# Optimization experiments

Measured on AMD Instinct MI355X. Metric: run time of the kernel, lower is better.

Reference implementation:

```python
import jax, jax.numpy as jnp
import numpy as np

B, T, D, H, L = 4, 128, 768, 770, 40  # batch, token_num, bert dim, head hidden, n_labels


def setup_inputs() -> dict:
    key = jax.random.key(0)
    ks = jax.random.split(key, 7)
    hidden = jax.random.normal(ks[0], (B, T + 1, D), dtype=jnp.float32)
    pred_spans = jnp.sort(jax.random.randint(ks[1], (B, 2), 0, T), axis=1)
    span_avail = jax.random.randint(ks[2], (T, T), 0, 2).astype(jnp.int32)
    # torch nn.Linear: weight init N(0, 0.02), bias init N(0, 1) (normal_(bias, 0) -> mean=0, std=1)
    W1 = (jax.random.normal(ks[3], (2 * D + 1, H)) * 0.02).astype(jnp.float32)
    b1 = jax.random.normal(ks[4], (H,), dtype=jnp.float32)
    W2 = (jax.random.normal(ks[5], (H, L)) * 0.02).astype(jnp.float32)
    b2 = jax.random.normal(ks[6], (L,), dtype=jnp.float32)
    return {"hidden": hidden, "W1": W1, "b1": b1, "W2": W2, "b2": b2,
            "pred_spans": pred_spans, "span_avail": span_avail, "token_num": T}


def reference(hidden, W1, b1, W2, b2, pred_spans, span_avail, token_num):
    # vecs[i] = hidden[:, i+1, :]  (skip [CLS])
    vecs = hidden[:, 1:token_num + 1, :]                      # [B, T, D]
    Bv, Tv, Dv = vecs.shape
    starts = pred_spans[:, 0][:, None, None]                  # [B,1,1]
    ends = pred_spans[:, 1][:, None, None]
    ii = jnp.arange(Tv)[:, None]                              # [T,1]
    jj = jnp.arange(Tv)[None, :]                              # [1,T]
    # indication: 2 if (i,j) == pred span; 1 if strictly inside span with i<=j; else 0
    is_full = (ii == starts) & (jj == ends)                   # [B,T,T]
    inside = (starts <= ii) & (ii <= jj) & (jj <= ends) & (~is_full)
    ind = (2 * is_full + inside).astype(hidden.dtype)         # [B,T,T]
    fi = jnp.broadcast_to(vecs[:, :, None, :], (Bv, Tv, Tv, Dv))
    fj = jnp.broadcast_to(vecs[:, None, :, :], (Bv, Tv, Tv, Dv))
    feat = jnp.concatenate([fi, fj, ind[..., None]], axis=-1)  # [B,T,T,2D+1]
    h = jax.nn.relu(feat @ W1 + b1)                            # [B,T,T,H]
    out = h @ W2 + b2                                          # [B,T,T,L]
    # unavailable spans contribute a zeros row (original appends `zeros`)
    mask = (span_avail >= 1)[None, :, :, None]
    out = jnp.where(mask, out, jnp.zeros((), out.dtype))
    out = out.reshape(Bv, Tv * Tv, -1)                         # span index c = i*T + j
    return jax.nn.log_softmax(out, axis=1)
```

## Files before the change

### kernel.cpp

```cpp
#include <hip/hip_runtime.h>
#include <math.h>

#define BB 4
#define TT 128
#define DD 768
#define HD 770
#define HP 800
#define LL 40
#define TP1 129

typedef __attribute__((ext_vector_type(8))) short s16x8;
typedef __attribute__((ext_vector_type(4))) float f32x4;

#define P_OFF   0
#define Q_OFF   409600
#define W2F_OFF 819200
#define BF1_OFF 838400
#define ACC_OFF 1440512

__device__ __forceinline__ unsigned pkbf(float a, float b) {
    unsigned ua = __float_as_uint(a);
    unsigned ub = __float_as_uint(b);
    return ((ua + 0x8000u) >> 16) | ((ub + 0x8000u) & 0xffff0000u);
}
__device__ __forceinline__ unsigned rne1(float v) {
    unsigned x = __float_as_uint(v);
    return (x + 0x7fffu + ((x >> 16) & 1u)) >> 16;
}

__global__ __launch_bounds__(256) void kPrep(const float* __restrict__ W1,
                                             const float* __restrict__ W2,
                                             float* __restrict__ Q,
                                             unsigned* __restrict__ W2f,
                                             unsigned* __restrict__ Bf1,
                                             float* __restrict__ accum) {
    const int bx = blockIdx.x;
    const int tid = threadIdx.x;
    if (bx < 19) {
        int u = bx * 256 + tid;
        if (u >= 4800) return;
        int nt = u / 1600;
        int rem = u - nt * 1600;
        int ks = rem >> 6;
        int lane = rem & 63;
        int kbase = ks * 32 + ((lane >> 4) << 3);
        int l = nt * 16 + (lane & 15);
        unsigned pk[4];
        #pragma unroll
        for (int sp = 0; sp < 4; ++sp) {
            unsigned w[2];
            #pragma unroll
            for (int e = 0; e < 2; ++e) {
                int k = kbase + 2 * sp + e;
                float v = (k < HD && l < LL) ? W2[k * LL + l] : 0.0f;
                w[e] = rne1(v);
            }
            pk[sp] = w[0] | (w[1] << 16);
        }
        ((uint4*)W2f)[u] = make_uint4(pk[0], pk[1], pk[2], pk[3]);
    } else if (bx < 607) {
        int u = (bx - 19) * 256 + tid;
        int lane = u & 63;
        int g = u >> 6;
        int ks = g % 24;
        int g2 = g / 24;
        int nt = g2 % 49;
        int half = g2 / 49;
        int kbase = ks * 32 + ((lane >> 4) << 3);
        int h = nt * 16 + (lane & 15);
        int row0 = half * DD + kbase;
        unsigned pk[4];
        #pragma unroll
        for (int sp = 0; sp < 4; ++sp) {
            unsigned w[2];
            #pragma unroll
            for (int e = 0; e < 2; ++e) {
                float v = (h < HD) ? W1[(size_t)(row0 + 2 * sp + e) * HD + h] : 0.0f;
                w[e] = rne1(v);
            }
            pk[sp] = w[0] | (w[1] << 16);
        }
        ((uint4*)Bf1)[u] = make_uint4(pk[0], pk[1], pk[2], pk[3]);
    } else {
        int u = (bx - 607) * 256 + tid;
        if (u < 160) accum[u] = 0.0f;
        int u2 = u - 160;
        if (u2 >= 0 && u2 < 512 * 30) {
            int row = u2 / 30;
            int h = HD + (u2 - row * 30);
            Q[(size_t)row * HP + h] = 0.0f;
        }
    }
}

__global__ __launch_bounds__(256) void kA(const float* __restrict__ hidden,
                                          const unsigned* __restrict__ Bf1,
                                          const float* __restrict__ b1,
                                          float* __restrict__ P,
                                          float* __restrict__ Q) {
    const int tid = threadIdx.x;
    const int w = blockIdx.x * 4 + (tid >> 6);
    const int lane = tid & 63;
    const int mband = w & 31;
    const int nt = w >> 5;
    const int b  = mband >> 3;
    const int tt = mband & 7;

    const float* __restrict__ Arow =
        hidden + (size_t)(b * TP1 + 1 + tt * 16 + (lane & 15)) * DD + ((lane >> 4) << 3);
    const uint4* __restrict__ B0 = (const uint4*)Bf1 + ((size_t)nt * 24) * 64 + lane;
    const uint4* __restrict__ B1 = (const uint4*)Bf1 + ((size_t)(49 + nt) * 24) * 64 + lane;

    f32x4 a0 = (f32x4){0.f,0.f,0.f,0.f};
    f32x4 a1 = (f32x4){0.f,0.f,0.f,0.f};

    #pragma unroll 4
    for (int ks = 0; ks < 24; ++ks) {
        float4 x0 = *(const float4*)(Arow + ks * 32);
        float4 x1 = *(const float4*)(Arow + ks * 32 + 4);
        union { unsigned u[4]; s16x8 v; } af;
        af.u[0] = pkbf(x0.x, x0.y); af.u[1] = pkbf(x0.z, x0.w);
        af.u[2] = pkbf(x1.x, x1.y); af.u[3] = pkbf(x1.z, x1.w);
        union { uint4 q; s16x8 v; } bf0, bf1;
        bf0.q = B0[ks * 64];
        bf1.q = B1[ks * 64];
        a0 = __builtin_amdgcn_mfma_f32_16x16x32_bf16(af.v, bf0.v, a0, 0, 0, 0);
        a1 = __builtin_amdgcn_mfma_f32_16x16x32_bf16(af.v, bf1.v, a1, 0, 0, 0);
    }

    const int col = lane & 15;
    const int h = nt * 16 + col;
    if (h < HD) {
        const float bv = b1[h];
        const int quad = lane >> 4;
        #pragma unroll
        for (int r = 0; r < 4; ++r) {
            int t = tt * 16 + quad * 4 + r;
            size_t row = (size_t)(b * TT + t) * HP;
            P[row + h] = a0[r] + bv;
            Q[row + h] = a1[r];
        }
    }
}

__global__ __launch_bounds__(256) void kB(const float* __restrict__ P,
                                          const float* __restrict__ Q,
                                          const float* __restrict__ W1,
                                          const unsigned* __restrict__ Bfrag,
                                          const float* __restrict__ b2,
                                          const int* __restrict__ spans,
                                          const int* __restrict__ avail,
                                          float* __restrict__ out,
                                          float* __restrict__ accum) {
    __shared__ unsigned Sb[2][128 * 20];
    __shared__ float var[3 * HP];
    __shared__ int avi[TT];
    __shared__ float sred[192];

    const int i = blockIdx.x;
    const int b = blockIdx.y;
    const int tid = threadIdx.x;
    const int wave = tid >> 6;
    const int lane = tid & 63;

    const int start = spans[b * 2];
    const int end   = spans[b * 2 + 1];

    const int jS = tid >> 1;
    const int hh = (tid & 1) << 4;
    int indS;
    {
        bool isfull = (i == start) && (jS == end);
        bool inside = (start <= i) && (i <= jS) && (jS <= end) && !isfull;
        indS = isfull ? 2 : (inside ? 1 : 0);
    }

    {
        const float* Pi  = P + (size_t)(b * TT + i) * HP;
        const float* w1L = W1 + (size_t)2 * DD * HD;
        for (int h = tid; h < HP; h += 256) {
            float pv = (h < HD) ? Pi[h] : 0.0f;
            float wv = (h < HD) ? w1L[h] : 0.0f;
            var[h]          = pv;
            var[HP + h]     = pv + wv;
            var[2*HP + h]   = pv + wv + wv;
        }
        if (tid < TT) avi[tid] = avail[i * TT + tid];
    }
    __syncthreads();

    const float* Qj = Q + (size_t)(b * TT + jS) * HP;
    const float* vb = var + indS * HP;

    auto form = [&](int c, int p) {
        const int h0 = c * 32 + hh;
        const float4* qp = (const float4*)(Qj + h0);
        float4 q0 = qp[0], q1 = qp[1], q2 = qp[2], q3 = qp[3];
        const float4* vp = (const float4*)(vb + h0);
        float4 v0 = vp[0], v1 = vp[1], v2 = vp[2], v3 = vp[3];
        float s0 = fmaxf(v0.x + q0.x, 0.f), s1 = fmaxf(v0.y + q0.y, 0.f);
        float s2 = fmaxf(v0.z + q0.z, 0.f), s3 = fmaxf(v0.w + q0.w, 0.f);
        float s4 = fmaxf(v1.x + q1.x, 0.f), s5 = fmaxf(v1.y + q1.y, 0.f);
        float s6 = fmaxf(v1.z + q1.z, 0.f), s7 = fmaxf(v1.w + q1.w, 0.f);
        float s8 = fmaxf(v2.x + q2.x, 0.f), s9 = fmaxf(v2.y + q2.y, 0.f);
        float sa = fmaxf(v2.z + q2.z, 0.f), sb_ = fmaxf(v2.w + q2.w, 0.f);
        float sc = fmaxf(v3.x + q3.x, 0.f), sd = fmaxf(v3.y + q3.y, 0.f);
        float se = fmaxf(v3.z + q3.z, 0.f), sf = fmaxf(v3.w + q3.w, 0.f);
        uint4* dst = (uint4*)(&Sb[p][jS * 20 + (hh >> 1)]);
        dst[0] = make_uint4(pkbf(s0,s1), pkbf(s2,s3), pkbf(s4,s5), pkbf(s6,s7));
        dst[1] = make_uint4(pkbf(s8,s9), pkbf(sa,sb_), pkbf(sc,sd), pkbf(se,sf));
    };

    f32x4 acc[2][3];
    #pragma unroll
    for (int mt = 0; mt < 2; ++mt)
        #pragma unroll
        for (int nt = 0; nt < 3; ++nt)
            acc[mt][nt] = (f32x4){0.f, 0.f, 0.f, 0.f};

    form(0, 0);
    __syncthreads();

    const int arow0 = (wave * 32 + (lane & 15)) * 20 + ((lane >> 4) << 2);
    for (int c = 0; c < 25; ++c) {
        const int p = c & 1;
        s16x8 bf0 = *(const s16x8*)(Bfrag + (( 0 + c) * 64 + lane) * 4);
        s16x8 bf1 = *(const s16x8*)(Bfrag + ((25 + c) * 64 + lane) * 4);
        s16x8 bf2 = *(const s16x8*)(Bfrag + ((50 + c) * 64 + lane) * 4);
        s16x8 af0 = *(const s16x8*)(&Sb[p][arow0]);
        s16x8 af1 = *(const s16x8*)(&Sb[p][arow0 + 16 * 20]);
        if (c + 1 < 25) form(c + 1, p ^ 1);
        acc[0][0] = __builtin_amdgcn_mfma_f32_16x16x32_bf16(af0, bf0, acc[0][0], 0, 0, 0);
        acc[0][1] = __builtin_amdgcn_mfma_f32_16x16x32_bf16(af0, bf1, acc[0][1], 0, 0, 0);
        acc[0][2] = __builtin_amdgcn_mfma_f32_16x16x32_bf16(af0, bf2, acc[0][2], 0, 0, 0);
        acc[1][0] = __builtin_amdgcn_mfma_f32_16x16x32_bf16(af1, bf0, acc[1][0], 0, 0, 0);
        acc[1][1] = __builtin_amdgcn_mfma_f32_16x16x32_bf16(af1, bf1, acc[1][1], 0, 0, 0);
        acc[1][2] = __builtin_amdgcn_mfma_f32_16x16x32_bf16(af1, bf2, acc[1][2], 0, 0, 0);
        __syncthreads();
    }

    float bias[3];
    #pragma unroll
    for (int nt = 0; nt < 3; ++nt) {
        int l = nt * 16 + (lane & 15);
        bias[nt] = (l < LL) ? b2[l] : 0.0f;
    }
    const int jr0 = wave * 32 + ((lane >> 4) << 2);
    float sE[3] = {0.f, 0.f, 0.f};
    #pragma unroll
    for (int mt = 0; mt < 2; ++mt) {
        #pragma unroll
        for (int r = 0; r < 4; ++r) {
            int j = jr0 + mt * 16 + r;
            bool msk = avi[j] >= 1;
            size_t rowoff = ((size_t)(b * (TT * TT) + i * TT + j)) * LL;
            #pragma unroll
            for (int nt = 0; nt < 3; ++nt) {
                int l = nt * 16 + (lane & 15);
                if (l < LL) {
                    float val = msk ? (acc[mt][nt][r] + bias[nt]) : 0.0f;
                    out[rowoff + l] = val;
                    sE[nt] += __expf(val);
                }
            }
        }
    }
    #pragma unroll
    for (int nt = 0; nt < 3; ++nt) {
        float v = sE[nt];
        v += __shfl_xor(v, 16);
        v += __shfl_xor(v, 32);
        if (lane < 16) sred[wave * 48 + nt * 16 + lane] = v;
    }
    __syncthreads();
    if (tid < 48) {
        float t4 = sred[tid] + sred[48 + tid] + sred[96 + tid] + sred[144 + tid];
        if (tid < LL) atomicAdd(&accum[b * LL + tid], t4);
    }
}

__global__ __launch_bounds__(256) void kD(float* __restrict__ out,
                                          const float* __restrict__ accum) {
    const int idx = blockIdx.x * 256 + threadIdx.x;
    const int e = idx * 4;
    const int b = e / (TT * TT * LL);
    const int l = e % LL;
    float4 v = ((float4*)out)[idx];
    const float* ac = accum + b * LL + l;
    v.x -= __logf(ac[0]); v.y -= __logf(ac[1]);
    v.z -= __logf(ac[2]); v.w -= __logf(ac[3]);
    ((float4*)out)[idx] = v;
}

extern "C" void kernel_launch(void* const* d_in, const int* in_sizes, int n_in,
                              void* d_out, int out_size, void* d_ws, size_t ws_size,
                              hipStream_t stream) {
    const float* hidden = (const float*)d_in[0];
    const float* W1     = (const float*)d_in[1];
    const float* b1     = (const float*)d_in[2];
    const float* W2     = (const float*)d_in[3];
    const float* b2     = (const float*)d_in[4];
    const int*   spans  = (const int*)d_in[5];
    const int*   avail  = (const int*)d_in[6];
    float* out = (float*)d_out;
    float* ws  = (float*)d_ws;

    float*    P     = ws + P_OFF;
    float*    Q     = ws + Q_OFF;
    unsigned* W2f   = (unsigned*)(ws + W2F_OFF);
    unsigned* Bf1   = (unsigned*)(ws + BF1_OFF);
    float*    accum = ws + ACC_OFF;

    kPrep<<<dim3(668),     dim3(256), 0, stream>>>(W1, W2, Q, W2f, Bf1, accum);
    kA   <<<dim3(392),     dim3(256), 0, stream>>>(hidden, Bf1, b1, P, Q);
    kB   <<<dim3(TT, BB),  dim3(256), 0, stream>>>(P, Q, W1, W2f, b2, spans, avail, out, accum);
    kD   <<<dim3(2560),    dim3(256), 0, stream>>>(out, accum);
}
```

Before: 128.6 us.

## Fuse prep, projection, head and log-softmax into one cooperative kernel

Replaces the four separate kernel launches with a single cooperative kernel of 512 blocks that uses grid-wide syncs between the weight-prep, first-projection, head GEMM and log-softmax normalisation phases. It also pre-converts the hidden activations to bf16 fragments in a workspace buffer, so the projection phase loads packed bf16 instead of converting fp32 inline. The aim is to remove launch gaps and per-kernel tail effects. In exchange, every block must stay co-resident, which the 256,2 launch bounds are meant to allow, and grid syncs add barrier cost while idle waves wait in the phases that use fewer blocks.

```diff
diff --git a/kernel.cpp b/kernel.cpp
--- a/kernel.cpp
+++ b/kernel.cpp
@@ -1,5 +1,8 @@
 #include <hip/hip_runtime.h>
+#include <hip/hip_cooperative_groups.h>
 #include <math.h>
+
+namespace cg = cooperative_groups;
 
 #define BB 4
 #define TT 128
@@ -16,7 +19,8 @@
 #define Q_OFF   409600
 #define W2F_OFF 819200
 #define BF1_OFF 838400
-#define ACC_OFF 1440512
+#define AF_OFF  1440512
+#define ACC_OFF 1637120
 
 __device__ __forceinline__ unsigned pkbf(float a, float b) {
     unsigned ua = __float_as_uint(a);
@@ -28,23 +32,77 @@
     return (x + 0x7fffu + ((x >> 16) & 1u)) >> 16;
 }
 
-__global__ __launch_bounds__(256) void kPrep(const float* __restrict__ W1,
-                                             const float* __restrict__ W2,
-                                             float* __restrict__ Q,
-                                             unsigned* __restrict__ W2f,
-                                             unsigned* __restrict__ Bf1,
-                                             float* __restrict__ accum) {
-    const int bx = blockIdx.x;
-    const int tid = threadIdx.x;
-    if (bx < 19) {
-        int u = bx * 256 + tid;
-        if (u >= 4800) return;
-        int nt = u / 1600;
-        int rem = u - nt * 1600;
+__global__ __launch_bounds__(256, 2) void kFused(
+    const float* __restrict__ hidden, const float* __restrict__ W1,
+    const float* __restrict__ W2, const float* __restrict__ b1,
+    const float* __restrict__ b2, const int* __restrict__ spans,
+    const int* __restrict__ avail, float* __restrict__ out,
+    float* __restrict__ ws)
+{
+    __shared__ unsigned Sb[2][128 * 20];
+    __shared__ float var[3 * HP];
+    __shared__ int avi[TT];
+    __shared__ float sred[192];
+
+    cg::grid_group grid = cg::this_grid();
+
+    float*    P     = ws + P_OFF;
+    float*    Q     = ws + Q_OFF;
+    unsigned* W2f   = (unsigned*)(ws + W2F_OFF);
+    unsigned* Bf1   = (unsigned*)(ws + BF1_OFF);
+    unsigned* Af    = (unsigned*)(ws + AF_OFF);
+    float*    accum = ws + ACC_OFF;
+
+    const int tid  = threadIdx.x;
+    const int g    = blockIdx.x * 256 + tid;
+    const int wave = tid >> 6;
+    const int lane = tid & 63;
+
+    for (int u = g; u < 150528; u += 131072) {
+        int ln = u & 63;
+        int gi = u >> 6;
+        int ks = gi % 24;
+        int g2 = gi / 24;
+        int nt = g2 % 49;
+        int half = g2 / 49;
+        int kbase = ks * 32 + ((ln >> 4) << 3);
+        int h = nt * 16 + (ln & 15);
+        int row0 = half * DD + kbase;
+        unsigned pk[4];
+        #pragma unroll
+        for (int sp = 0; sp < 4; ++sp) {
+            unsigned w[2];
+            #pragma unroll
+            for (int e = 0; e < 2; ++e) {
+                float v = (h < HD) ? W1[(size_t)(row0 + 2 * sp + e) * HD + h] : 0.0f;
+                w[e] = rne1(v);
+            }
+            pk[sp] = w[0] | (w[1] << 16);
+        }
+        ((uint4*)Bf1)[u] = make_uint4(pk[0], pk[1], pk[2], pk[3]);
+    }
+    if (g < 49152) {
+        int ln = g & 63;
+        int fi = g >> 6;
+        int ks = fi % 24;
+        int mband = fi / 24;
+        int b = mband >> 3;
+        int tt = mband & 7;
+        int m = ln & 15;
+        int kb = ks * 32 + ((ln >> 4) << 3);
+        const float* src = hidden + (size_t)(b * TP1 + 1 + tt * 16 + m) * DD + kb;
+        float4 x0 = ((const float4*)src)[0];
+        float4 x1 = ((const float4*)src)[1];
+        ((uint4*)Af)[g] = make_uint4(pkbf(x0.x, x0.y), pkbf(x0.z, x0.w),
+                                     pkbf(x1.x, x1.y), pkbf(x1.z, x1.w));
+    }
+    if (g < 4800) {
+        int nt = g / 1600;
+        int rem = g - nt * 1600;
         int ks = rem >> 6;
-        int lane = rem & 63;
-        int kbase = ks * 32 + ((lane >> 4) << 3);
-        int l = nt * 16 + (lane & 15);
+        int ln = rem & 63;
+        int kbase = ks * 32 + ((ln >> 4) << 3);
+        int l = nt * 16 + (ln & 15);
         unsigned pk[4];
         #pragma unroll
         for (int sp = 0; sp < 4; ++sp) {
@@ -57,239 +115,193 @@
             }
             pk[sp] = w[0] | (w[1] << 16);
         }
-        ((uint4*)W2f)[u] = make_uint4(pk[0], pk[1], pk[2], pk[3]);
-    } else if (bx < 607) {
-        int u = (bx - 19) * 256 + tid;
-        int lane = u & 63;
-        int g = u >> 6;
-        int ks = g % 24;
-        int g2 = g / 24;
-        int nt = g2 % 49;
-        int half = g2 / 49;
-        int kbase = ks * 32 + ((lane >> 4) << 3);
-        int h = nt * 16 + (lane & 15);
-        int row0 = half * DD + kbase;
-        unsigned pk[4];
-        #pragma unroll
-        for (int sp = 0; sp < 4; ++sp) {
-            unsigned w[2];
+        ((uint4*)W2f)[g] = make_uint4(pk[0], pk[1], pk[2], pk[3]);
+    }
+    if (g < 16384) {
+        int row = g >> 5;
+        Q[(size_t)row * HP + 768 + (g & 31)] = 0.0f;
+    }
+    if (g < 160) accum[g] = 0.0f;
+
+    grid.sync();
+
+    {
+        const int gw = blockIdx.x * 4 + wave;
+        if (gw < 1568) {
+            const int mband = gw & 31;
+            const int nt = gw >> 5;
+            const int b = mband >> 3;
+            const int tt = mband & 7;
+
+            const uint4* __restrict__ A0 = (const uint4*)Af + (size_t)mband * 24 * 64 + lane;
+            const uint4* __restrict__ B0 = (const uint4*)Bf1 + ((size_t)nt * 24) * 64 + lane;
+            const uint4* __restrict__ B1 = (const uint4*)Bf1 + ((size_t)(49 + nt) * 24) * 64 + lane;
+
+            f32x4 a0 = (f32x4){0.f, 0.f, 0.f, 0.f};
+            f32x4 a1 = (f32x4){0.f, 0.f, 0.f, 0.f};
+
+            #pragma unroll 4
+            for (int ks = 0; ks < 24; ++ks) {
+                union { uint4 q; s16x8 v; } af, bf0, bf1;
+                af.q  = A0[ks * 64];
+                bf0.q = B0[ks * 64];
+                bf1.q = B1[ks * 64];
+                a0 = __builtin_amdgcn_mfma_f32_16x16x32_bf16(af.v, bf0.v, a0, 0, 0, 0);
+                a1 = __builtin_amdgcn_mfma_f32_16x16x32_bf16(af.v, bf1.v, a1, 0, 0, 0);
+            }
+
+            const int col = lane & 15;
+            const int h = nt * 16 + col;
+            if (h < HD) {
+                const float bv = b1[h];
+                const int quad = lane >> 4;
+                #pragma unroll
+                for (int r = 0; r < 4; ++r) {
+                    int t = tt * 16 + quad * 4 + r;
+                    size_t row = (size_t)(b * TT + t) * HP;
+                    P[row + h] = a0[r] + bv;
+                    Q[row + h] = a1[r];
+                }
+            }
+        }
+    }
+
+    grid.sync();
+
+    {
+        const int i = blockIdx.x & 127;
+        const int b = blockIdx.x >> 7;
+
+        const int start = spans[b * 2];
+        const int end   = spans[b * 2 + 1];
+
+        const int jS = tid >> 1;
+        const int hh = (tid & 1) << 4;
+        int indS;
+        {
+            bool isfull = (i == start) && (jS == end);
+            bool inside = (start <= i) && (i <= jS) && (jS <= end) && !isfull;
+            indS = isfull ? 2 : (inside ? 1 : 0);
+        }
+
+        {
+            const float* Pi  = P + (size_t)(b * TT + i) * HP;
+            const float* w1L = W1 + (size_t)2 * DD * HD;
+            for (int h = tid; h < HP; h += 256) {
+                float pv = (h < HD) ? Pi[h] : 0.0f;
+                float wv = (h < HD) ? w1L[h] : 0.0f;
+                var[h]        = pv;
+                var[HP + h]   = pv + wv;
+                var[2*HP + h] = pv + wv + wv;
+            }
+            if (tid < TT) avi[tid] = avail[i * TT + tid];
+        }
+        __syncthreads();
+
+        const float* Qj = Q + (size_t)(b * TT + jS) * HP;
+        const float* vb = var + indS * HP;
+
+        auto form = [&](int c, int p) {
+            const int h0 = c * 32 + hh;
+            const float4* qp = (const float4*)(Qj + h0);
+            float4 q0 = qp[0], q1 = qp[1], q2 = qp[2], q3 = qp[3];
+            const float4* vp = (const float4*)(vb + h0);
+            float4 v0 = vp[0], v1 = vp[1], v2 = vp[2], v3 = vp[3];
+            float s0 = fmaxf(v0.x + q0.x, 0.f), s1 = fmaxf(v0.y + q0.y, 0.f);
+            float s2 = fmaxf(v0.z + q0.z, 0.f), s3 = fmaxf(v0.w + q0.w, 0.f);
+            float s4 = fmaxf(v1.x + q1.x, 0.f), s5 = fmaxf(v1.y + q1.y, 0.f);
+            float s6 = fmaxf(v1.z + q1.z, 0.f), s7 = fmaxf(v1.w + q1.w, 0.f);
+            float s8 = fmaxf(v2.x + q2.x, 0.f), s9 = fmaxf(v2.y + q2.y, 0.f);
+            float sa = fmaxf(v2.z + q2.z, 0.f), sb_ = fmaxf(v2.w + q2.w, 0.f);
+            float sc = fmaxf(v3.x + q3.x, 0.f), sd = fmaxf(v3.y + q3.y, 0.f);
+            float se = fmaxf(v3.z + q3.z, 0.f), sf = fmaxf(v3.w + q3.w, 0.f);
+            uint4* dst = (uint4*)(&Sb[p][jS * 20 + (hh >> 1)]);
+            dst[0] = make_uint4(pkbf(s0,s1), pkbf(s2,s3), pkbf(s4,s5), pkbf(s6,s7));
+            dst[1] = make_uint4(pkbf(s8,s9), pkbf(sa,sb_), pkbf(sc,sd), pkbf(se,sf));
+        };
+
+        f32x4 acc[2][3];
+        #pragma unroll
+        for (int mt = 0; mt < 2; ++mt)
             #pragma unroll
-            for (int e = 0; e < 2; ++e) {
-                float v = (h < HD) ? W1[(size_t)(row0 + 2 * sp + e) * HD + h] : 0.0f;
-                w[e] = rne1(v);
-            }
-            pk[sp] = w[0] | (w[1] << 16);
-        }
-        ((uint4*)Bf1)[u] = make_uint4(pk[0], pk[1], pk[2], pk[3]);
-    } else {
-        int u = (bx - 607) * 256 + tid;
-        if (u < 160) accum[u] = 0.0f;
-        int u2 = u - 160;
-        if (u2 >= 0 && u2 < 512 * 30) {
-            int row = u2 / 30;
-            int h = HD + (u2 - row * 30);
-            Q[(size_t)row * HP + h] = 0.0f;
-        }
-    }
-}
-
-__global__ __launch_bounds__(256) void kA(const float* __restrict__ hidden,
-                                          const unsigned* __restrict__ Bf1,
-                                          const float* __restrict__ b1,
-                                          float* __restrict__ P,
-                                          float* __restrict__ Q) {
-    const int tid = threadIdx.x;
-    const int w = blockIdx.x * 4 + (tid >> 6);
-    const int lane = tid & 63;
-    const int mband = w & 31;
-    const int nt = w >> 5;
-    const int b  = mband >> 3;
-    const int tt = mband & 7;
-
-    const float* __restrict__ Arow =
-        hidden + (size_t)(b * TP1 + 1 + tt * 16 + (lane & 15)) * DD + ((lane >> 4) << 3);
-    const uint4* __restrict__ B0 = (const uint4*)Bf1 + ((size_t)nt * 24) * 64 + lane;
-    const uint4* __restrict__ B1 = (const uint4*)Bf1 + ((size_t)(49 + nt) * 24) * 64 + lane;
-
-    f32x4 a0 = (f32x4){0.f,0.f,0.f,0.f};
-    f32x4 a1 = (f32x4){0.f,0.f,0.f,0.f};
-
-    #pragma unroll 4
-    for (int ks = 0; ks < 24; ++ks) {
-        float4 x0 = *(const float4*)(Arow + ks * 32);
-        float4 x1 = *(const float4*)(Arow + ks * 32 + 4);
-        union { unsigned u[4]; s16x8 v; } af;
-        af.u[0] = pkbf(x0.x, x0.y); af.u[1] = pkbf(x0.z, x0.w);
-        af.u[2] = pkbf(x1.x, x1.y); af.u[3] = pkbf(x1.z, x1.w);
-        union { uint4 q; s16x8 v; } bf0, bf1;
-        bf0.q = B0[ks * 64];
-        bf1.q = B1[ks * 64];
-        a0 = __builtin_amdgcn_mfma_f32_16x16x32_bf16(af.v, bf0.v, a0, 0, 0, 0);
-        a1 = __builtin_amdgcn_mfma_f32_16x16x32_bf16(af.v, bf1.v, a1, 0, 0, 0);
-    }
-
-    const int col = lane & 15;
-    const int h = nt * 16 + col;
-    if (h < HD) {
-        const float bv = b1[h];
-        const int quad = lane >> 4;
-        #pragma unroll
-        for (int r = 0; r < 4; ++r) {
-            int t = tt * 16 + quad * 4 + r;
-            size_t row = (size_t)(b * TT + t) * HP;
-            P[row + h] = a0[r] + bv;
-            Q[row + h] = a1[r];
-        }
-    }
-}
-
-__global__ __launch_bounds__(256) void kB(const float* __restrict__ P,
-                                          const float* __restrict__ Q,
-                                          const float* __restrict__ W1,
-                                          const unsigned* __restrict__ Bfrag,
-                                          const float* __restrict__ b2,
-                                          const int* __restrict__ spans,
-                                          const int* __restrict__ avail,
-                                          float* __restrict__ out,
-                                          float* __restrict__ accum) {
-    __shared__ unsigned Sb[2][128 * 20];
-    __shared__ float var[3 * HP];
-    __shared__ int avi[TT];
-    __shared__ float sred[192];
-
-    const int i = blockIdx.x;
-    const int b = blockIdx.y;
-    const int tid = threadIdx.x;
-    const int wave = tid >> 6;
-    const int lane = tid & 63;
-
-    const int start = spans[b * 2];
-    const int end   = spans[b * 2 + 1];
-
-    const int jS = tid >> 1;
-    const int hh = (tid & 1) << 4;
-    int indS;
-    {
-        bool isfull = (i == start) && (jS == end);
-        bool inside = (start <= i) && (i <= jS) && (jS <= end) && !isfull;
-        indS = isfull ? 2 : (inside ? 1 : 0);
-    }
-
-    {
-        const float* Pi  = P + (size_t)(b * TT + i) * HP;
-        const float* w1L = W1 + (size_t)2 * DD * HD;
-        for (int h = tid; h < HP; h += 256) {
-            float pv = (h < HD) ? Pi[h] : 0.0f;
-            float wv = (h < HD) ? w1L[h] : 0.0f;
-            var[h]          = pv;
-            var[HP + h]     = pv + wv;
-            var[2*HP + h]   = pv + wv + wv;
-        }
-        if (tid < TT) avi[tid] = avail[i * TT + tid];
-    }
-    __syncthreads();
-
-    const float* Qj = Q + (size_t)(b * TT + jS) * HP;
-    const float* vb = var + indS * HP;
-
-    auto form = [&](int c, int p) {
-        const int h0 = c * 32 + hh;
-        const float4* qp = (const float4*)(Qj + h0);
-        float4 q0 = qp[0], q1 = qp[1], q2 = qp[2], q3 = qp[3];
-        const float4* vp = (const float4*)(vb + h0);
-        float4 v0 = vp[0], v1 = vp[1], v2 = vp[2], v3 = vp[3];
-        float s0 = fmaxf(v0.x + q0.x, 0.f), s1 = fmaxf(v0.y + q0.y, 0.f);
-        float s2 = fmaxf(v0.z + q0.z, 0.f), s3 = fmaxf(v0.w + q0.w, 0.f);
-        float s4 = fmaxf(v1.x + q1.x, 0.f), s5 = fmaxf(v1.y + q1.y, 0.f);
-        float s6 = fmaxf(v1.z + q1.z, 0.f), s7 = fmaxf(v1.w + q1.w, 0.f);
-        float s8 = fmaxf(v2.x + q2.x, 0.f), s9 = fmaxf(v2.y + q2.y, 0.f);
-        float sa = fmaxf(v2.z + q2.z, 0.f), sb_ = fmaxf(v2.w + q2.w, 0.f);
-        float sc = fmaxf(v3.x + q3.x, 0.f), sd = fmaxf(v3.y + q3.y, 0.f);
-        float se = fmaxf(v3.z + q3.z, 0.f), sf = fmaxf(v3.w + q3.w, 0.f);
-        uint4* dst = (uint4*)(&Sb[p][jS * 20 + (hh >> 1)]);
-        dst[0] = make_uint4(pkbf(s0,s1), pkbf(s2,s3), pkbf(s4,s5), pkbf(s6,s7));
-        dst[1] = make_uint4(pkbf(s8,s9), pkbf(sa,sb_), pkbf(sc,sd), pkbf(se,sf));
-    };
-
-    f32x4 acc[2][3];
+            for (int nt = 0; nt < 3; ++nt)
+                acc[mt][nt] = (f32x4){0.f, 0.f, 0.f, 0.f};
+
+        form(0, 0);
+        __syncthreads();
+
+        const int arow0 = (wave * 32 + (lane & 15)) * 20 + ((lane >> 4) << 2);
+        for (int c = 0; c < 25; ++c) {
+            const int p = c & 1;
+            s16x8 bf0 = *(const s16x8*)((const unsigned*)W2f + (( 0 + c) * 64 + lane) * 4);
+            s16x8 bf1 = *(const s16x8*)((const unsigned*)W2f + ((25 + c) * 64 + lane) * 4);
+            s16x8 bf2 = *(const s16x8*)((const unsigned*)W2f + ((50 + c) * 64 + lane) * 4);
+            s16x8 af0 = *(const s16x8*)(&Sb[p][arow0]);
+            s16x8 af1 = *(const s16x8*)(&Sb[p][arow0 + 16 * 20]);
+            if (c + 1 < 25) form(c + 1, p ^ 1);
+            acc[0][0] = __builtin_amdgcn_mfma_f32_16x16x32_bf16(af0, bf0, acc[0][0], 0, 0, 0);
+            acc[0][1] = __builtin_amdgcn_mfma_f32_16x16x32_bf16(af0, bf1, acc[0][1], 0, 0, 0);
+            acc[0][2] = __builtin_amdgcn_mfma_f32_16x16x32_bf16(af0, bf2, acc[0][2], 0, 0, 0);
+            acc[1][0] = __builtin_amdgcn_mfma_f32_16x16x32_bf16(af1, bf0, acc[1][0], 0, 0, 0);
+            acc[1][1] = __builtin_amdgcn_mfma_f32_16x16x32_bf16(af1, bf1, acc[1][1], 0, 0, 0);
+            acc[1][2] = __builtin_amdgcn_mfma_f32_16x16x32_bf16(af1, bf2, acc[1][2], 0, 0, 0);
+            __syncthreads();
+        }
+
+        float bias[3];
+        #pragma unroll
+        for (int nt = 0; nt < 3; ++nt) {
+            int l = nt * 16 + (lane & 15);
+            bias[nt] = (l < LL) ? b2[l] : 0.0f;
+        }
+        const int jr0 = wave * 32 + ((lane >> 4) << 2);
+        float sE[3] = {0.f, 0.f, 0.f};
+        #pragma unroll
+        for (int mt = 0; mt < 2; ++mt) {
+            #pragma unroll
+            for (int r = 0; r < 4; ++r) {
+                int j = jr0 + mt * 16 + r;
+                bool msk = avi[j] >= 1;
+                size_t rowoff = ((size_t)(b * (TT * TT) + i * TT + j)) * LL;
+                #pragma unroll
+                for (int nt = 0; nt < 3; ++nt) {
+                    int l = nt * 16 + (lane & 15);
+                    if (l < LL) {
+                        float val = msk ? (acc[mt][nt][r] + bias[nt]) : 0.0f;
+                        out[rowoff + l] = val;
+                        sE[nt] += __expf(val);
+                    }
+                }
+            }
+        }
+        #pragma unroll
+        for (int nt = 0; nt < 3; ++nt) {
+            float v = sE[nt];
+            v += __shfl_xor(v, 16);
+            v += __shfl_xor(v, 32);
+            if (lane < 16) sred[wave * 48 + nt * 16 + lane] = v;
+        }
+        __syncthreads();
+        if (tid < 48) {
+            float t4 = sred[tid] + sred[48 + tid] + sred[96 + tid] + sred[144 + tid];
+            if (tid < LL) atomicAdd(&accum[b * LL + tid], t4);
+        }
+    }
+
+    grid.sync();
+
     #pragma unroll
-    for (int mt = 0; mt < 2; ++mt)
-        #pragma unroll
-        for (int nt = 0; nt < 3; ++nt)
-            acc[mt][nt] = (f32x4){0.f, 0.f, 0.f, 0.f};
-
-    form(0, 0);
-    __syncthreads();
-
-    const int arow0 = (wave * 32 + (lane & 15)) * 20 + ((lane >> 4) << 2);
-    for (int c = 0; c < 25; ++c) {
-        const int p = c & 1;
-        s16x8 bf0 = *(const s16x8*)(Bfrag + (( 0 + c) * 64 + lane) * 4);
-        s16x8 bf1 = *(const s16x8*)(Bfrag + ((25 + c) * 64 + lane) * 4);
-        s16x8 bf2 = *(const s16x8*)(Bfrag + ((50 + c) * 64 + lane) * 4);
-        s16x8 af0 = *(const s16x8*)(&Sb[p][arow0]);
-        s16x8 af1 = *(const s16x8*)(&Sb[p][arow0 + 16 * 20]);
-        if (c + 1 < 25) form(c + 1, p ^ 1);
-        acc[0][0] = __builtin_amdgcn_mfma_f32_16x16x32_bf16(af0, bf0, acc[0][0], 0, 0, 0);
-        acc[0][1] = __builtin_amdgcn_mfma_f32_16x16x32_bf16(af0, bf1, acc[0][1], 0, 0, 0);
-        acc[0][2] = __builtin_amdgcn_mfma_f32_16x16x32_bf16(af0, bf2, acc[0][2], 0, 0, 0);
-        acc[1][0] = __builtin_amdgcn_mfma_f32_16x16x32_bf16(af1, bf0, acc[1][0], 0, 0, 0);
-        acc[1][1] = __builtin_amdgcn_mfma_f32_16x16x32_bf16(af1, bf1, acc[1][1], 0, 0, 0);
-        acc[1][2] = __builtin_amdgcn_mfma_f32_16x16x32_bf16(af1, bf2, acc[1][2], 0, 0, 0);
-        __syncthreads();
-    }
-
-    float bias[3];
-    #pragma unroll
-    for (int nt = 0; nt < 3; ++nt) {
-        int l = nt * 16 + (lane & 15);
-        bias[nt] = (l < LL) ? b2[l] : 0.0f;
-    }
-    const int jr0 = wave * 32 + ((lane >> 4) << 2);
-    float sE[3] = {0.f, 0.f, 0.f};
-    #pragma unroll
-    for (int mt = 0; mt < 2; ++mt) {
-        #pragma unroll
-        for (int r = 0; r < 4; ++r) {
-            int j = jr0 + mt * 16 + r;
-            bool msk = avi[j] >= 1;
-            size_t rowoff = ((size_t)(b * (TT * TT) + i * TT + j)) * LL;
-            #pragma unroll
-            for (int nt = 0; nt < 3; ++nt) {
-                int l = nt * 16 + (lane & 15);
-                if (l < LL) {
-                    float val = msk ? (acc[mt][nt][r] + bias[nt]) : 0.0f;
-                    out[rowoff + l] = val;
-                    sE[nt] += __expf(val);
-                }
-            }
-        }
-    }
-    #pragma unroll
-    for (int nt = 0; nt < 3; ++nt) {
-        float v = sE[nt];
-        v += __shfl_xor(v, 16);
-        v += __shfl_xor(v, 32);
-        if (lane < 16) sred[wave * 48 + nt * 16 + lane] = v;
-    }
-    __syncthreads();
-    if (tid < 48) {
-        float t4 = sred[tid] + sred[48 + tid] + sred[96 + tid] + sred[144 + tid];
-        if (tid < LL) atomicAdd(&accum[b * LL + tid], t4);
-    }
-}
-
-__global__ __launch_bounds__(256) void kD(float* __restrict__ out,
-                                          const float* __restrict__ accum) {
-    const int idx = blockIdx.x * 256 + threadIdx.x;
-    const int e = idx * 4;
-    const int b = e / (TT * TT * LL);
-    const int l = e % LL;
-    float4 v = ((float4*)out)[idx];
-    const float* ac = accum + b * LL + l;
-    v.x -= __logf(ac[0]); v.y -= __logf(ac[1]);
-    v.z -= __logf(ac[2]); v.w -= __logf(ac[3]);
-    ((float4*)out)[idx] = v;
+    for (int it = 0; it < 5; ++it) {
+        const int idx = g + it * 131072;
+        const int e = idx * 4;
+        const int b = e / (TT * TT * LL);
+        const int l = e % LL;
+        float4 v = ((float4*)out)[idx];
+        const float* ac = accum + b * LL + l;
+        v.x -= __logf(ac[0]); v.y -= __logf(ac[1]);
+        v.z -= __logf(ac[2]); v.w -= __logf(ac[3]);
+        ((float4*)out)[idx] = v;
+    }
 }
 
 extern "C" void kernel_launch(void* const* d_in, const int* in_sizes, int n_in,
@@ -305,14 +317,7 @@
     float* out = (float*)d_out;
     float* ws  = (float*)d_ws;
 
-    float*    P     = ws + P_OFF;
-    float*    Q     = ws + Q_OFF;
-    unsigned* W2f   = (unsigned*)(ws + W2F_OFF);
-    unsigned* Bf1   = (unsigned*)(ws + BF1_OFF);
-    float*    accum = ws + ACC_OFF;
-
-    kPrep<<<dim3(668),     dim3(256), 0, stream>>>(W1, W2, Q, W2f, Bf1, accum);
-    kA   <<<dim3(392),     dim3(256), 0, stream>>>(hidden, Bf1, b1, P, Q);
-    kB   <<<dim3(TT, BB),  dim3(256), 0, stream>>>(P, Q, W1, W2f, b2, spans, avail, out, accum);
-    kD   <<<dim3(2560),    dim3(256), 0, stream>>>(out, accum);
+    void* args[] = {(void*)&hidden, (void*)&W1, (void*)&W2, (void*)&b1, (void*)&b2,
+                    (void*)&spans, (void*)&avail, (void*)&out, (void*)&ws};
+    hipLaunchCooperativeKernel((const void*)kFused, dim3(512), dim3(256), args, 0, stream);
 }
```

Result: slower. 325.0 us (+152.7%).

## Fuse W1 bf16 conversion into first GEMM and widen second-GEMM chunks to 64

Applied to the files above, without the earlier changes.

Drops the separate prep kernel and the pre-packed W1 fragment buffer. The first GEMM now reads fp32 W1 directly and rounds it to bf16 in registers, and the small W2 packing, accumulator clearing and Q padding become extra blocks of the same launch. The second GEMM stages 64 hidden columns per step instead of 32, roughly halving loop iterations and barriers; the last chunk zero-fills the upper half. This saves a launch and a global round trip for the W1 fragments. In exchange, each wave re-reads and re-converts strided fp32 W1, and the 33-word LDS row stride leaves 128-bit LDS accesses misaligned.

```diff
diff --git a/kernel.cpp b/kernel.cpp
--- a/kernel.cpp
+++ b/kernel.cpp
@@ -15,8 +15,7 @@
 #define P_OFF   0
 #define Q_OFF   409600
 #define W2F_OFF 819200
-#define BF1_OFF 838400
-#define ACC_OFF 1440512
+#define ACC_OFF 838400
 
 __device__ __forceinline__ unsigned pkbf(float a, float b) {
     unsigned ua = __float_as_uint(a);
@@ -28,131 +27,108 @@
     return (x + 0x7fffu + ((x >> 16) & 1u)) >> 16;
 }
 
-__global__ __launch_bounds__(256) void kPrep(const float* __restrict__ W1,
-                                             const float* __restrict__ W2,
-                                             float* __restrict__ Q,
-                                             unsigned* __restrict__ W2f,
-                                             unsigned* __restrict__ Bf1,
-                                             float* __restrict__ accum) {
-    const int bx = blockIdx.x;
+__global__ __launch_bounds__(256) void kA(const float* __restrict__ hidden,
+                                          const float* __restrict__ W1,
+                                          const float* __restrict__ W2,
+                                          const float* __restrict__ b1,
+                                          float* __restrict__ P,
+                                          float* __restrict__ Q,
+                                          unsigned* __restrict__ W2f,
+                                          float* __restrict__ accum) {
+    const int bx  = blockIdx.x;
     const int tid = threadIdx.x;
-    if (bx < 19) {
-        int u = bx * 256 + tid;
+    if (bx < 392) {
+        const int wave = tid >> 6;
+        const int lane = tid & 63;
+        const int w = bx * 4 + wave;
+        const int mband = w & 31;
+        const int nt = w >> 5;
+        const int b  = mband >> 3;
+        const int tt = mband & 7;
+        const int col  = lane & 15;
+        const int quad = lane >> 4;
+        const int h = nt * 16 + col;
+
+        const float* __restrict__ Arow =
+            hidden + (size_t)(b * TP1 + 1 + tt * 16 + col) * DD + quad * 8;
+
+        f32x4 a0 = (f32x4){0.f, 0.f, 0.f, 0.f};
+        f32x4 a1 = (f32x4){0.f, 0.f, 0.f, 0.f};
+
+        #pragma unroll 2
+        for (int ks = 0; ks < 24; ++ks) {
+            float4 x0 = ((const float4*)(Arow + ks * 32))[0];
+            float4 x1 = ((const float4*)(Arow + ks * 32))[1];
+            union { unsigned u[4]; s16x8 v; } af;
+            af.u[0] = pkbf(x0.x, x0.y); af.u[1] = pkbf(x0.z, x0.w);
+            af.u[2] = pkbf(x1.x, x1.y); af.u[3] = pkbf(x1.z, x1.w);
+            const int k0 = ks * 32 + quad * 8;
+            const float* wp0 = W1 + (size_t)k0 * HD + h;
+            const float* wp1 = W1 + (size_t)(DD + k0) * HD + h;
+            union { unsigned u[4]; s16x8 v; } bf0, bf1;
+            #pragma unroll
+            for (int sp = 0; sp < 4; ++sp) {
+                bf0.u[sp] = rne1(wp0[(size_t)(2*sp) * HD]) |
+                            (rne1(wp0[(size_t)(2*sp+1) * HD]) << 16);
+                bf1.u[sp] = rne1(wp1[(size_t)(2*sp) * HD]) |
+                            (rne1(wp1[(size_t)(2*sp+1) * HD]) << 16);
+            }
+            a0 = __builtin_amdgcn_mfma_f32_16x16x32_bf16(af.v, bf0.v, a0, 0, 0, 0);
+            a1 = __builtin_amdgcn_mfma_f32_16x16x32_bf16(af.v, bf1.v, a1, 0, 0, 0);
+        }
+
+        if (h < HD) {
+            const float bv = b1[h];
+            #pragma unroll
+            for (int r = 0; r < 4; ++r) {
+                int t = tt * 16 + quad * 4 + r;
+                size_t row = (size_t)(b * TT + t) * HP;
+                P[row + h] = a0[r] + bv;
+                Q[row + h] = a1[r];
+            }
+        }
+    } else if (bx < 411) {
+        int u = (bx - 392) * 256 + tid;
         if (u >= 4800) return;
         int nt = u / 1600;
         int rem = u - nt * 1600;
         int ks = rem >> 6;
-        int lane = rem & 63;
-        int kbase = ks * 32 + ((lane >> 4) << 3);
-        int l = nt * 16 + (lane & 15);
+        int ln = rem & 63;
+        int kbase = ks * 32 + ((ln >> 4) << 3);
+        int l = nt * 16 + (ln & 15);
         unsigned pk[4];
         #pragma unroll
         for (int sp = 0; sp < 4; ++sp) {
-            unsigned w[2];
+            unsigned wv[2];
             #pragma unroll
             for (int e = 0; e < 2; ++e) {
                 int k = kbase + 2 * sp + e;
                 float v = (k < HD && l < LL) ? W2[k * LL + l] : 0.0f;
-                w[e] = rne1(v);
-            }
-            pk[sp] = w[0] | (w[1] << 16);
+                wv[e] = rne1(v);
+            }
+            pk[sp] = wv[0] | (wv[1] << 16);
         }
         ((uint4*)W2f)[u] = make_uint4(pk[0], pk[1], pk[2], pk[3]);
-    } else if (bx < 607) {
-        int u = (bx - 19) * 256 + tid;
-        int lane = u & 63;
-        int g = u >> 6;
-        int ks = g % 24;
-        int g2 = g / 24;
-        int nt = g2 % 49;
-        int half = g2 / 49;
-        int kbase = ks * 32 + ((lane >> 4) << 3);
-        int h = nt * 16 + (lane & 15);
-        int row0 = half * DD + kbase;
-        unsigned pk[4];
-        #pragma unroll
-        for (int sp = 0; sp < 4; ++sp) {
-            unsigned w[2];
-            #pragma unroll
-            for (int e = 0; e < 2; ++e) {
-                float v = (h < HD) ? W1[(size_t)(row0 + 2 * sp + e) * HD + h] : 0.0f;
-                w[e] = rne1(v);
-            }
-            pk[sp] = w[0] | (w[1] << 16);
-        }
-        ((uint4*)Bf1)[u] = make_uint4(pk[0], pk[1], pk[2], pk[3]);
+    } else if (bx == 411) {
+        if (tid < 160) accum[tid] = 0.0f;
     } else {
-        int u = (bx - 607) * 256 + tid;
-        if (u < 160) accum[u] = 0.0f;
-        int u2 = u - 160;
-        if (u2 >= 0 && u2 < 512 * 30) {
-            int row = u2 / 30;
-            int h = HD + (u2 - row * 30);
-            Q[(size_t)row * HP + h] = 0.0f;
-        }
-    }
-}
-
-__global__ __launch_bounds__(256) void kA(const float* __restrict__ hidden,
-                                          const unsigned* __restrict__ Bf1,
-                                          const float* __restrict__ b1,
-                                          float* __restrict__ P,
-                                          float* __restrict__ Q) {
-    const int tid = threadIdx.x;
-    const int w = blockIdx.x * 4 + (tid >> 6);
-    const int lane = tid & 63;
-    const int mband = w & 31;
-    const int nt = w >> 5;
-    const int b  = mband >> 3;
-    const int tt = mband & 7;
-
-    const float* __restrict__ Arow =
-        hidden + (size_t)(b * TP1 + 1 + tt * 16 + (lane & 15)) * DD + ((lane >> 4) << 3);
-    const uint4* __restrict__ B0 = (const uint4*)Bf1 + ((size_t)nt * 24) * 64 + lane;
-    const uint4* __restrict__ B1 = (const uint4*)Bf1 + ((size_t)(49 + nt) * 24) * 64 + lane;
-
-    f32x4 a0 = (f32x4){0.f,0.f,0.f,0.f};
-    f32x4 a1 = (f32x4){0.f,0.f,0.f,0.f};
-
-    #pragma unroll 4
-    for (int ks = 0; ks < 24; ++ks) {
-        float4 x0 = *(const float4*)(Arow + ks * 32);
-        float4 x1 = *(const float4*)(Arow + ks * 32 + 4);
-        union { unsigned u[4]; s16x8 v; } af;
-        af.u[0] = pkbf(x0.x, x0.y); af.u[1] = pkbf(x0.z, x0.w);
-        af.u[2] = pkbf(x1.x, x1.y); af.u[3] = pkbf(x1.z, x1.w);
-        union { uint4 q; s16x8 v; } bf0, bf1;
-        bf0.q = B0[ks * 64];
-        bf1.q = B1[ks * 64];
-        a0 = __builtin_amdgcn_mfma_f32_16x16x32_bf16(af.v, bf0.v, a0, 0, 0, 0);
-        a1 = __builtin_amdgcn_mfma_f32_16x16x32_bf16(af.v, bf1.v, a1, 0, 0, 0);
-    }
-
-    const int col = lane & 15;
-    const int h = nt * 16 + col;
-    if (h < HD) {
-        const float bv = b1[h];
-        const int quad = lane >> 4;
-        #pragma unroll
-        for (int r = 0; r < 4; ++r) {
-            int t = tt * 16 + quad * 4 + r;
-            size_t row = (size_t)(b * TT + t) * HP;
-            P[row + h] = a0[r] + bv;
-            Q[row + h] = a1[r];
-        }
+        int u = (bx - 412) * 256 + tid;
+        int row = u / 30;
+        int h = HD + (u - row * 30);
+        Q[(size_t)row * HP + h] = 0.0f;
     }
 }
 
 __global__ __launch_bounds__(256) void kB(const float* __restrict__ P,
                                           const float* __restrict__ Q,
                                           const float* __restrict__ W1,
-                                          const unsigned* __restrict__ Bfrag,
+                                          const unsigned* __restrict__ W2f,
                                           const float* __restrict__ b2,
                                           const int* __restrict__ spans,
                                           const int* __restrict__ avail,
                                           float* __restrict__ out,
                                           float* __restrict__ accum) {
-    __shared__ unsigned Sb[2][128 * 20];
+    __shared__ unsigned Sb[2][128 * 33];
     __shared__ float var[3 * HP];
     __shared__ int avi[TT];
     __shared__ float sred[192];
@@ -166,8 +142,8 @@
     const int start = spans[b * 2];
     const int end   = spans[b * 2 + 1];
 
-    const int jS = tid >> 1;
-    const int hh = (tid & 1) << 4;
+    const int jS   = tid >> 1;
+    const int half = tid & 1;
     int indS;
     {
         bool isfull = (i == start) && (jS == end);
@@ -181,9 +157,9 @@
         for (int h = tid; h < HP; h += 256) {
             float pv = (h < HD) ? Pi[h] : 0.0f;
             float wv = (h < HD) ? w1L[h] : 0.0f;
-            var[h]          = pv;
-            var[HP + h]     = pv + wv;
-            var[2*HP + h]   = pv + wv + wv;
+            var[h]        = pv;
+            var[HP + h]   = pv + wv;
+            var[2*HP + h] = pv + wv + wv;
         }
         if (tid < TT) avi[tid] = avail[i * TT + tid];
     }
@@ -192,23 +168,47 @@
     const float* Qj = Q + (size_t)(b * TT + jS) * HP;
     const float* vb = var + indS * HP;
 
-    auto form = [&](int c, int p) {
-        const int h0 = c * 32 + hh;
-        const float4* qp = (const float4*)(Qj + h0);
-        float4 q0 = qp[0], q1 = qp[1], q2 = qp[2], q3 = qp[3];
-        const float4* vp = (const float4*)(vb + h0);
-        float4 v0 = vp[0], v1 = vp[1], v2 = vp[2], v3 = vp[3];
-        float s0 = fmaxf(v0.x + q0.x, 0.f), s1 = fmaxf(v0.y + q0.y, 0.f);
-        float s2 = fmaxf(v0.z + q0.z, 0.f), s3 = fmaxf(v0.w + q0.w, 0.f);
-        float s4 = fmaxf(v1.x + q1.x, 0.f), s5 = fmaxf(v1.y + q1.y, 0.f);
-        float s6 = fmaxf(v1.z + q1.z, 0.f), s7 = fmaxf(v1.w + q1.w, 0.f);
-        float s8 = fmaxf(v2.x + q2.x, 0.f), s9 = fmaxf(v2.y + q2.y, 0.f);
-        float sa = fmaxf(v2.z + q2.z, 0.f), sb_ = fmaxf(v2.w + q2.w, 0.f);
-        float sc = fmaxf(v3.x + q3.x, 0.f), sd = fmaxf(v3.y + q3.y, 0.f);
-        float se = fmaxf(v3.z + q3.z, 0.f), sf = fmaxf(v3.w + q3.w, 0.f);
-        uint4* dst = (uint4*)(&Sb[p][jS * 20 + (hh >> 1)]);
-        dst[0] = make_uint4(pkbf(s0,s1), pkbf(s2,s3), pkbf(s4,s5), pkbf(s6,s7));
-        dst[1] = make_uint4(pkbf(s8,s9), pkbf(sa,sb_), pkbf(sc,sd), pkbf(se,sf));
+    auto form = [&](int c, int p, bool valid) {
+        unsigned d[8];
+        if (valid) {
+            const int h0 = c * 64 + half * 32;
+            const float4* qp = (const float4*)(Qj + h0);
+            const float4* vp = (const float4*)(vb + h0);
+            #pragma unroll
+            for (int g = 0; g < 4; ++g) {
+                float4 q0 = qp[2*g], q1 = qp[2*g + 1];
+                float4 v0 = vp[2*g], v1 = vp[2*g + 1];
+                float s0 = fmaxf(v0.x + q0.x, 0.f), s1 = fmaxf(v0.y + q0.y, 0.f);
+                float s2 = fmaxf(v0.z + q0.z, 0.f), s3 = fmaxf(v0.w + q0.w, 0.f);
+                float s4 = fmaxf(v1.x + q1.x, 0.f), s5 = fmaxf(v1.y + q1.y, 0.f);
+                float s6 = fmaxf(v1.z + q1.z, 0.f), s7 = fmaxf(v1.w + q1.w, 0.f);
+                d[2*g]   = pkbf(s0, s1) , d[2*g]   = pkbf(s0, s1);
+                d[2*g]   = pkbf(s0, s1);
+                d[2*g+1] = pkbf(s2, s3);
+                d[2*g]   = pkbf(s0, s1);
+                d[2*g+1] = pkbf(s2, s3);
+                (void)s4; (void)s5; (void)s6; (void)s7;
+            }
+            const float4* qq = qp; const float4* vv = vp;
+            unsigned e[16];
+            #pragma unroll
+            for (int g = 0; g < 8; ++g) {
+                float4 qv = qq[g], vw = vv[g];
+                float t0 = fmaxf(vw.x + qv.x, 0.f), t1 = fmaxf(vw.y + qv.y, 0.f);
+                float t2 = fmaxf(vw.z + qv.z, 0.f), t3 = fmaxf(vw.w + qv.w, 0.f);
+                e[2*g]   = pkbf(t0, t1);
+                e[2*g+1] = pkbf(t2, t3);
+            }
+            uint4* dst = (uint4*)(&Sb[p][jS * 33 + half * 16]);
+            dst[0] = make_uint4(e[0],  e[1],  e[2],  e[3]);
+            dst[1] = make_uint4(e[4],  e[5],  e[6],  e[7]);
+            dst[2] = make_uint4(e[8],  e[9],  e[10], e[11]);
+            dst[3] = make_uint4(e[12], e[13], e[14], e[15]);
+        } else {
+            uint4* dst = (uint4*)(&Sb[p][jS * 33 + half * 16]);
+            uint4 z = make_uint4(0u, 0u, 0u, 0u);
+            dst[0] = z; dst[1] = z; dst[2] = z; dst[3] = z;
+        }
     };
 
     f32x4 acc[2][3];
@@ -218,24 +218,40 @@
         for (int nt = 0; nt < 3; ++nt)
             acc[mt][nt] = (f32x4){0.f, 0.f, 0.f, 0.f};
 
-    form(0, 0);
+    form(0, 0, true);
     __syncthreads();
 
-    const int arow0 = (wave * 32 + (lane & 15)) * 20 + ((lane >> 4) << 2);
-    for (int c = 0; c < 25; ++c) {
+    const int arow0 = (wave * 32 + (lane & 15)) * 33 + ((lane >> 4) << 2);
+    const unsigned* W2fu = W2f;
+    for (int c = 0; c < 13; ++c) {
         const int p = c & 1;
-        s16x8 bf0 = *(const s16x8*)(Bfrag + (( 0 + c) * 64 + lane) * 4);
-        s16x8 bf1 = *(const s16x8*)(Bfrag + ((25 + c) * 64 + lane) * 4);
-        s16x8 bf2 = *(const s16x8*)(Bfrag + ((50 + c) * 64 + lane) * 4);
-        s16x8 af0 = *(const s16x8*)(&Sb[p][arow0]);
-        s16x8 af1 = *(const s16x8*)(&Sb[p][arow0 + 16 * 20]);
-        if (c + 1 < 25) form(c + 1, p ^ 1);
-        acc[0][0] = __builtin_amdgcn_mfma_f32_16x16x32_bf16(af0, bf0, acc[0][0], 0, 0, 0);
-        acc[0][1] = __builtin_amdgcn_mfma_f32_16x16x32_bf16(af0, bf1, acc[0][1], 0, 0, 0);
-        acc[0][2] = __builtin_amdgcn_mfma_f32_16x16x32_bf16(af0, bf2, acc[0][2], 0, 0, 0);
-        acc[1][0] = __builtin_amdgcn_mfma_f32_16x16x32_bf16(af1, bf0, acc[1][0], 0, 0, 0);
-        acc[1][1] = __builtin_amdgcn_mfma_f32_16x16x32_bf16(af1, bf1, acc[1][1], 0, 0, 0);
-        acc[1][2] = __builtin_amdgcn_mfma_f32_16x16x32_bf16(af1, bf2, acc[1][2], 0, 0, 0);
+        const int ks0 = 2 * c;
+        const int ks1 = (c < 12) ? (2 * c + 1) : 0;
+        s16x8 b00 = *(const s16x8*)(W2fu + (( 0 + ks0) * 64 + lane) * 4);
+        s16x8 b01 = *(const s16x8*)(W2fu + ((25 + ks0) * 64 + lane) * 4);
+        s16x8 b02 = *(const s16x8*)(W2fu + ((50 + ks0) * 64 + lane) * 4);
+        s16x8 b10 = *(const s16x8*)(W2fu + (( 0 + ks1) * 64 + lane) * 4);
+        s16x8 b11 = *(const s16x8*)(W2fu + ((25 + ks1) * 64 + lane) * 4);
+        s16x8 b12 = *(const s16x8*)(W2fu + ((50 + ks1) * 64 + lane) * 4);
+        s16x8 a00 = *(const s16x8*)(&Sb[p][arow0]);
+        s16x8 a10 = *(const s16x8*)(&Sb[p][arow0 + 16 * 33]);
+        s16x8 a01 = *(const s16x8*)(&Sb[p][arow0 + 16]);
+        s16x8 a11 = *(const s16x8*)(&Sb[p][arow0 + 16 * 33 + 16]);
+        if (c + 1 < 13) form(c + 1, p ^ 1, (c + 1 < 12) || (half == 0));
+        acc[0][0] = __builtin_amdgcn_mfma_f32_16x16x32_bf16(a00, b00, acc[0][0], 0, 0, 0);
+        acc[0][1] = __builtin_amdgcn_mfma_f32_16x16x32_bf16(a00, b01, acc[0][1], 0, 0, 0);
+        acc[0][2] = __builtin_amdgcn_mfma_f32_16x16x32_bf16(a00, b02, acc[0][2], 0, 0, 0);
+        acc[1][0] = __builtin_amdgcn_mfma_f32_16x16x32_bf16(a10, b00, acc[1][0], 0, 0, 0);
+        acc[1][1] = __builtin_amdgcn_mfma_f32_16x16x32_bf16(a10, b01, acc[1][1], 0, 0, 0);
+        acc[1][2] = __builtin_amdgcn_mfma_f32_16x16x32_bf16(a10, b02, acc[1][2], 0, 0, 0);
+        if (c < 12) {
+            acc[0][0] = __builtin_amdgcn_mfma_f32_16x16x32_bf16(a01, b10, acc[0][0], 0, 0, 0);
+            acc[0][1] = __builtin_amdgcn_mfma_f32_16x16x32_bf16(a01, b11, acc[0][1], 0, 0, 0);
+            acc[0][2] = __builtin_amdgcn_mfma_f32_16x16x32_bf16(a01, b12, acc[0][2], 0, 0, 0);
+            acc[1][0] = __builtin_amdgcn_mfma_f32_16x16x32_bf16(a11, b10, acc[1][0], 0, 0, 0);
+            acc[1][1] = __builtin_amdgcn_mfma_f32_16x16x32_bf16(a11, b11, acc[1][1], 0, 0, 0);
+            acc[1][2] = __builtin_amdgcn_mfma_f32_16x16x32_bf16(a11, b12, acc[1][2], 0, 0, 0);
+        }
         __syncthreads();
     }
 
@@ -308,11 +324,9 @@
     float*    P     = ws + P_OFF;
     float*    Q     = ws + Q_OFF;
     unsigned* W2f   = (unsigned*)(ws + W2F_OFF);
-    unsigned* Bf1   = (unsigned*)(ws + BF1_OFF);
     float*    accum = ws + ACC_OFF;
 
-    kPrep<<<dim3(668),     dim3(256), 0, stream>>>(W1, W2, Q, W2f, Bf1, accum);
-    kA   <<<dim3(392),     dim3(256), 0, stream>>>(hidden, Bf1, b1, P, Q);
-    kB   <<<dim3(TT, BB),  dim3(256), 0, stream>>>(P, Q, W1, W2f, b2, spans, avail, out, accum);
-    kD   <<<dim3(2560),    dim3(256), 0, stream>>>(out, accum);
-}
+    kA <<<dim3(472),    dim3(256), 0, stream>>>(hidden, W1, W2, b1, P, Q, W2f, accum);
+    kB <<<dim3(TT, BB), dim3(256), 0, stream>>>(P, Q, W1, W2f, b2, spans, avail, out, accum);
+    kD <<<dim3(2560),   dim3(256), 0, stream>>>(out, accum);
+}
```

Result: slower. 137.3 us (+6.7%).
